# Kernel tuning notes

Hardware: AMD Instinct MI355X
Metric: run time of the kernel (lower is better)

## Reference

```python
import jax, jax.numpy as jnp
import numpy as np

N, E, F, H = 50000, 1_600_000, 6, 64


def setup_inputs() -> dict:
    key = jax.random.key(0)
    ks = jax.random.split(key, 12)
    inp = {
        "vertex_features": jax.random.normal(ks[0], (N, F), dtype=jnp.float32),
        "edges": jax.random.randint(ks[1], (2, E), 0, N, dtype=jnp.int64 if jax.config.jax_enable_x64 else jnp.int32),
        "weights": jax.random.uniform(ks[2], (E,), dtype=jnp.float32),
        # GCNConv layer params (glorot-ish scale) + biases (PyG default bias=True)
        "W1": jax.random.normal(ks[3], (F, H), dtype=jnp.float32) / np.sqrt(F),
        "b1": jnp.zeros((H,), jnp.float32),
        "W2": jax.random.normal(ks[4], (H, H), dtype=jnp.float32) / np.sqrt(H),
        "b2": jnp.zeros((H,), jnp.float32),
        "W3": jax.random.normal(ks[5], (H, H), dtype=jnp.float32) / np.sqrt(H),
        "b3": jnp.zeros((H,), jnp.float32),
        "Wl": jax.random.normal(ks[6], (H, 1), dtype=jnp.float32) / np.sqrt(H),
        "bl": jnp.zeros((1,), jnp.float32),
    }
    return inp


def _gcn_norm(edges, weights, n):
    # PyG gcn_norm: add self loops (weight 1), symmetric D^-1/2 A D^-1/2;
    # degree computed at target nodes (edge_index[1], flow source_to_target).
    row, col = edges[0], edges[1]
    loop = jnp.arange(n, dtype=row.dtype)
    row_f = jnp.concatenate([row, loop])
    col_f = jnp.concatenate([col, loop])
    w_f = jnp.concatenate([weights, jnp.ones((n,), weights.dtype)])
    deg = jax.ops.segment_sum(w_f, col_f, num_segments=n)
    dis = jnp.where(deg > 0, jax.lax.rsqrt(jnp.maximum(deg, 1e-30)), 0.0)
    norm = dis[row_f] * w_f * dis[col_f]
    return row_f, col_f, norm


def _gcn_conv(x, W, b, row, col, norm, n):
    xw = x @ W                                   # [n, H_out]
    agg = jax.ops.segment_sum(norm[:, None] * xw[row], col, num_segments=n)
    return agg + b


def reference(vertex_features, edges, weights, W1, b1, W2, b2, W3, b3, Wl, bl):
    n = vertex_features.shape[0]
    row, col, norm = _gcn_norm(edges, weights, n)  # norm identical for all layers
    h = jax.nn.sigmoid(_gcn_conv(vertex_features, W1, b1, row, col, norm, n))
    h = jax.nn.sigmoid(_gcn_conv(h, W2, b2, row, col, norm, n))
    h = jax.nn.sigmoid(_gcn_conv(h, W3, b3, row, col, norm, n))
    logits = h @ Wl + bl                           # [n, 1]
    return jax.nn.softmax(logits, axis=0)          # softmax over node dim
```

## Files before the change

### kernel.cpp

```cpp
#include <hip/hip_runtime.h>
#include <math.h>


#define BLK 256
#define SKB 256
#define CHUNK 4096

typedef __attribute__((ext_vector_type(8))) short bf16x8;
typedef __attribute__((ext_vector_type(4))) float f32x4;

__device__ inline unsigned short f2bf(float f) {
  unsigned u = __float_as_uint(f);
  return (unsigned short)((u + 0x7FFF + ((u >> 16) & 1)) >> 16);
}
__device__ inline float bflo(unsigned u) { return __uint_as_float(u << 16); }
__device__ inline float bfhi(unsigned u) { return __uint_as_float(u & 0xFFFF0000u); }


__global__ __launch_bounds__(256) void k_binscatter(
    const int* __restrict__ row, const int* __restrict__ col,
    const float* __restrict__ w, int E,
    int* __restrict__ bfill, int2* __restrict__ bucket, int CAP) {
  __shared__ int2 stage[CHUNK];
  __shared__ int lhist[SKB], lbase[SKB], gbase[SKB], lfill[SKB];
  int t = threadIdx.x;
  int e0 = blockIdx.x * CHUNK;
  int n = E - e0; if (n > CHUNK) n = CHUNK;
  lhist[t] = 0; lfill[t] = 0;
  __syncthreads();
  for (int i = t; i < n; i += BLK) atomicAdd(&lhist[((unsigned)col[e0 + i]) >> 8], 1);
  __syncthreads();
  lbase[t] = lhist[t];
  __syncthreads();
  for (int off = 1; off < SKB; off <<= 1) {
    int v = (t >= off) ? lbase[t - off] : 0;
    __syncthreads();
    lbase[t] += v;
    __syncthreads();
  }
  int excl = lbase[t] - lhist[t];
  int cb = lhist[t];
  gbase[t] = cb ? atomicAdd(&bfill[t << 4], cb) : 0;
  __syncthreads();
  lbase[t] = excl;
  __syncthreads();
  for (int i = t; i < n; i += BLK) {
    int c = col[e0 + i];
    int b = ((unsigned)c) >> 8;
    int r = atomicAdd(&lfill[b], 1);
    stage[lbase[b] + r] = make_int2(row[e0 + i] | (c << 16), __float_as_int(w[e0 + i]));
  }
  __syncthreads();
  for (int i = t; i < n; i += BLK) {
    int2 p = stage[i];
    int b = ((unsigned)p.x) >> 24;
    bucket[(size_t)b * CAP + gbase[b] + (i - lbase[b])] = p;
  }
}


__global__ __launch_bounds__(256) void k_build(
    const int2* __restrict__ bucket, const int* __restrict__ bfill,
    const float* __restrict__ x,
    unsigned* __restrict__ csr, int* __restrict__ cnt, int* __restrict__ start,
    float* __restrict__ dis, float* __restrict__ x8p, int CAP, int N) {
  __shared__ int   hist[SKB];
  __shared__ float wsum[SKB];
  __shared__ int   lstart[SKB + 1];
  __shared__ int   lfill[SKB];
  int b = blockIdx.x, t = threadIdx.x;
  int n0 = b << 8;
  int M = N - n0; if (M > 256) M = 256;
  if (M <= 0) return;
  hist[t] = 0; wsum[t] = 0.0f; lfill[t] = 0;
  __syncthreads();
  const int2* bb = bucket + (size_t)b * CAP;
  int ec = bfill[b << 4];
  for (int i = t; i < ec; i += BLK) {
    int2 p = bb[i];
    int lc = (((unsigned)p.x) >> 16) & 255;
    atomicAdd(&hist[lc], 1);
    atomicAdd(&wsum[lc], __int_as_float(p.y));
  }
  __syncthreads();
  if (t == 0) {
    int run = 0;
    for (int i = 0; i < M; ++i) { lstart[i] = run; run += hist[i]; }
    lstart[M] = run;
  }
  __syncthreads();
  if (t < M) {
    int n = n0 + t;
    cnt[n] = hist[t];
    start[n] = b * CAP + lstart[t];
    float d = 1.0f / sqrtf(wsum[t] + 1.0f);
    dis[n] = d;
    const float* xr = x + (size_t)n * 6;
    float* xo = x8p + (size_t)n * 8;
#pragma unroll
    for (int k = 0; k < 6; ++k) xo[k] = d * xr[k];
    xo[6] = 0.0f; xo[7] = 0.0f;
  }
  __syncthreads();
  for (int i = t; i < ec; i += BLK) {
    int2 p = bb[i];
    int lc = (((unsigned)p.x) >> 16) & 255;
    int pos = lstart[lc] + atomicAdd(&lfill[lc], 1);
    csr[(size_t)b * CAP + pos] =
        ((unsigned)p.x & 0xFFFFu) | ((unsigned)f2bf(__int_as_float(p.y)) << 16);
  }
}


__global__ void k_wprep(const float* __restrict__ W2, const float* __restrict__ W3,
                        unsigned short* __restrict__ W2b, unsigned short* __restrict__ W3b) {
  int i = blockIdx.x * blockDim.x + threadIdx.x;
  if (i < 4096) { W2b[i] = f2bf(W2[i]); W3b[i] = f2bf(W3[i]); }
}


__global__ void k_layer1(const float* __restrict__ x8p,
                         const int* __restrict__ start, const int* __restrict__ cnt,
                         const unsigned* __restrict__ csr, const float* __restrict__ dis,
                         const float* __restrict__ W1, const float* __restrict__ b1,
                         unsigned short* __restrict__ hb, int N) {
  int n = blockIdx.x * blockDim.x + threadIdx.x;
  if (n >= N) return;
  const float4* xr = (const float4*)(x8p + (size_t)n * 8);
  float4 lo = xr[0], hi = xr[1];
  int s = start[n], e = s + cnt[n];
  for (int i = s; i < e; ++i) {
    unsigned pe = csr[i];
    float v = bfhi(pe);
    const float4* sr = (const float4*)(x8p + (size_t)(pe & 0xFFFFu) * 8);
    float4 a = sr[0], b = sr[1];
    lo.x += v * a.x; lo.y += v * a.y; lo.z += v * a.z; lo.w += v * a.w;
    hi.x += v * b.x; hi.y += v * b.y;
  }
  float d = dis[n];
  float a0 = d * lo.x, a1 = d * lo.y, a2 = d * lo.z, a3 = d * lo.w;
  float a4 = d * hi.x, a5 = d * hi.y;
  unsigned short* o = hb + (size_t)n * 64;
#pragma unroll
  for (int j4 = 0; j4 < 16; ++j4) {
    float4 acc = *(const float4*)(b1 + j4 * 4);
    const float* Wc = W1 + j4 * 4;
    acc.x += a0*Wc[0] + a1*Wc[64] + a2*Wc[128] + a3*Wc[192] + a4*Wc[256] + a5*Wc[320];
    acc.y += a0*Wc[1] + a1*Wc[65] + a2*Wc[129] + a3*Wc[193] + a4*Wc[257] + a5*Wc[321];
    acc.z += a0*Wc[2] + a1*Wc[66] + a2*Wc[130] + a3*Wc[194] + a4*Wc[258] + a5*Wc[322];
    acc.w += a0*Wc[3] + a1*Wc[67] + a2*Wc[131] + a3*Wc[195] + a4*Wc[259] + a5*Wc[323];
    uint2 pk;
    pk.x = (unsigned)f2bf(d / (1.0f + expf(-acc.x))) |
           ((unsigned)f2bf(d / (1.0f + expf(-acc.y))) << 16);
    pk.y = (unsigned)f2bf(d / (1.0f + expf(-acc.z))) |
           ((unsigned)f2bf(d / (1.0f + expf(-acc.w))) << 16);
    *(uint2*)(o + j4 * 4) = pk;
  }
}


__global__ void k_agg64(const unsigned short* __restrict__ hb,
                        const int* __restrict__ start, const int* __restrict__ cnt,
                        const unsigned* __restrict__ csr, const float* __restrict__ dis,
                        unsigned short* __restrict__ aggb, int N) {
  int t = blockIdx.x * blockDim.x + threadIdx.x;
  int n = t >> 3, sub = t & 7;
  if (n >= N) return;
  uint4 sv = *(const uint4*)(hb + (size_t)n * 64 + sub * 8);
  float a0 = bflo(sv.x), a1 = bfhi(sv.x), a2 = bflo(sv.y), a3 = bfhi(sv.y);
  float a4 = bflo(sv.z), a5 = bfhi(sv.z), a6 = bflo(sv.w), a7 = bfhi(sv.w);
  int s = start[n], e = s + cnt[n];
  for (int i = s; i < e; ++i) {
    unsigned pe = csr[i];
    float v = bfhi(pe);
    uint4 hv = *(const uint4*)(hb + (size_t)(pe & 0xFFFFu) * 64 + sub * 8);
    a0 += v * bflo(hv.x); a1 += v * bfhi(hv.x);
    a2 += v * bflo(hv.y); a3 += v * bfhi(hv.y);
    a4 += v * bflo(hv.z); a5 += v * bfhi(hv.z);
    a6 += v * bflo(hv.w); a7 += v * bfhi(hv.w);
  }
  float d = dis[n];
  uint4 pk;
  pk.x = (unsigned)f2bf(d * a0) | ((unsigned)f2bf(d * a1) << 16);
  pk.y = (unsigned)f2bf(d * a2) | ((unsigned)f2bf(d * a3) << 16);
  pk.z = (unsigned)f2bf(d * a4) | ((unsigned)f2bf(d * a5) << 16);
  pk.w = (unsigned)f2bf(d * a6) | ((unsigned)f2bf(d * a7) << 16);
  *(uint4*)(aggb + (size_t)n * 64 + sub * 8) = pk;
}


__global__ __launch_bounds__(256) void k_dense64_mfma(
    const unsigned short* __restrict__ aggb, const unsigned short* __restrict__ Wb,
    const float* __restrict__ b, const float* __restrict__ dis,
    unsigned short* __restrict__ hb, int NS) {
  int wid = threadIdx.x >> 6, lane = threadIdx.x & 63;
  int quad = lane >> 4, r16 = lane & 15;
  bf16x8 Bf[2][4];
#pragma unroll
  for (int kt = 0; kt < 2; ++kt)
#pragma unroll
    for (int jt = 0; jt < 4; ++jt)
#pragma unroll
      for (int j = 0; j < 8; ++j)
        Bf[kt][jt][j] = (short)Wb[(kt * 32 + quad * 8 + j) * 64 + jt * 16 + r16];
  float bias[4];
#pragma unroll
  for (int jt = 0; jt < 4; ++jt) bias[jt] = b[jt * 16 + r16];
  int stride = gridDim.x * 4;
  for (int s = blockIdx.x * 4 + wid; s < NS; s += stride) {
    int n0 = s * 16;
    bf16x8 Af0 = *(const bf16x8*)(aggb + (size_t)(n0 + r16) * 64 + quad * 8);
    bf16x8 Af1 = *(const bf16x8*)(aggb + (size_t)(n0 + r16) * 64 + 32 + quad * 8);
    f32x4 C[4];
#pragma unroll
    for (int jt = 0; jt < 4; ++jt) {
      f32x4 z = {0.f, 0.f, 0.f, 0.f};
      z = __builtin_amdgcn_mfma_f32_16x16x32_bf16(Af0, Bf[0][jt], z, 0, 0, 0);
      z = __builtin_amdgcn_mfma_f32_16x16x32_bf16(Af1, Bf[1][jt], z, 0, 0, 0);
      C[jt] = z;
    }
    float dv[4];
#pragma unroll
    for (int reg = 0; reg < 4; ++reg) dv[reg] = dis[n0 + quad * 4 + reg];
#pragma unroll
    for (int jt = 0; jt < 4; ++jt)
#pragma unroll
      for (int reg = 0; reg < 4; ++reg) {
        float h = dv[reg] / (1.0f + expf(-(C[jt][reg] + bias[jt])));
        hb[(size_t)(n0 + quad * 4 + reg) * 64 + jt * 16 + r16] = f2bf(h);
      }
  }
}


__global__ __launch_bounds__(256) void k_head_mfma(
    const unsigned short* __restrict__ aggb, const unsigned short* __restrict__ Wb,
    const float* __restrict__ b, const float* __restrict__ Wl,
    const float* __restrict__ bl, float* __restrict__ expv,
    float* __restrict__ red_part, int NS) {
  int wid = threadIdx.x >> 6, lane = threadIdx.x & 63;
  int quad = lane >> 4, r16 = lane & 15;
  bf16x8 Bf[2][4];
#pragma unroll
  for (int kt = 0; kt < 2; ++kt)
#pragma unroll
    for (int jt = 0; jt < 4; ++jt)
#pragma unroll
      for (int j = 0; j < 8; ++j)
        Bf[kt][jt][j] = (short)Wb[(kt * 32 + quad * 8 + j) * 64 + jt * 16 + r16];
  float bias[4], wlv[4];
#pragma unroll
  for (int jt = 0; jt < 4; ++jt) {
    bias[jt] = b[jt * 16 + r16];
    wlv[jt]  = Wl[jt * 16 + r16];
  }
  float bl0 = bl[0];
  float lsum = 0.0f;
  int stride = gridDim.x * 4;
  for (int s = blockIdx.x * 4 + wid; s < NS; s += stride) {
    int n0 = s * 16;
    bf16x8 Af0 = *(const bf16x8*)(aggb + (size_t)(n0 + r16) * 64 + quad * 8);
    bf16x8 Af1 = *(const bf16x8*)(aggb + (size_t)(n0 + r16) * 64 + 32 + quad * 8);
    f32x4 C[4];
#pragma unroll
    for (int jt = 0; jt < 4; ++jt) {
      f32x4 z = {0.f, 0.f, 0.f, 0.f};
      z = __builtin_amdgcn_mfma_f32_16x16x32_bf16(Af0, Bf[0][jt], z, 0, 0, 0);
      z = __builtin_amdgcn_mfma_f32_16x16x32_bf16(Af1, Bf[1][jt], z, 0, 0, 0);
      C[jt] = z;
    }
    float p0 = 0, p1 = 0, p2 = 0, p3 = 0;
#pragma unroll
    for (int jt = 0; jt < 4; ++jt) {
      p0 += wlv[jt] / (1.0f + expf(-(C[jt][0] + bias[jt])));
      p1 += wlv[jt] / (1.0f + expf(-(C[jt][1] + bias[jt])));
      p2 += wlv[jt] / (1.0f + expf(-(C[jt][2] + bias[jt])));
      p3 += wlv[jt] / (1.0f + expf(-(C[jt][3] + bias[jt])));
    }
#pragma unroll
    for (int m = 1; m < 16; m <<= 1) {
      p0 += __shfl_xor(p0, m, 64);
      p1 += __shfl_xor(p1, m, 64);
      p2 += __shfl_xor(p2, m, 64);
      p3 += __shfl_xor(p3, m, 64);
    }
    float ls = 0.0f;
    if (r16 == 0) {
      float e0 = expf(p0 + bl0), e1 = expf(p1 + bl0);
      float e2 = expf(p2 + bl0), e3 = expf(p3 + bl0);
      int r = n0 + quad * 4;
      expv[r] = e0; expv[r + 1] = e1; expv[r + 2] = e2; expv[r + 3] = e3;
      ls = e0 + e1 + e2 + e3;
    }
    ls += __shfl_xor(ls, 16, 64);
    ls += __shfl_xor(ls, 32, 64);
    lsum += ls;
  }
  if (lane == 0) atomicAdd(&red_part[(blockIdx.x & 63) << 4], lsum);
}

__global__ void k_out(const float* __restrict__ expv, int N,
                      const float* __restrict__ red_part, float* __restrict__ out) {
  int i = blockIdx.x * blockDim.x + threadIdx.x;
  int lane = threadIdx.x & 63;
  float s = red_part[lane << 4];
#pragma unroll
  for (int o = 32; o > 0; o >>= 1) s += __shfl_down(s, o, 64);
  s = __shfl(s, 0, 64);
  if (i < N) out[i] = expv[i] / s;
}


extern "C" void kernel_launch(void* const* d_in, const int* in_sizes, int n_in,
                              void* d_out, int out_size, void* d_ws, size_t ws_size,
                              hipStream_t stream) {
  const float* x   = (const float*)d_in[0];
  const int*   edg = (const int*)d_in[1];
  const float* w   = (const float*)d_in[2];
  const float* W1  = (const float*)d_in[3];
  const float* b1  = (const float*)d_in[4];
  const float* W2  = (const float*)d_in[5];
  const float* b2  = (const float*)d_in[6];
  const float* W3  = (const float*)d_in[7];
  const float* b3  = (const float*)d_in[8];
  const float* Wl  = (const float*)d_in[9];
  const float* bl  = (const float*)d_in[10];
  float* out = (float*)d_out;

  const int N = in_sizes[0] / 6;
  const int E = in_sizes[2];
  const int* row = edg;
  const int* col = edg + E;
  const int NB = (N + 255) >> 8;
  const int NS = (N + 15) / 16;

  size_t off = 0;
  char* base = (char*)d_ws;
  auto alloc = [&](size_t bytes) -> void* {
    void* p = base + off;
    off += (bytes + 255) & ~(size_t)255;
    return p;
  };
  int*   bfill    = (int*)alloc((size_t)SKB * 16 * 4);
  float* red_part = (float*)alloc((size_t)64 * 16 * 4);
  size_t zero_bytes = off;
  int*   cnt    = (int*)alloc((size_t)N * 4);
  int*   start  = (int*)alloc((size_t)N * 4);
  float* dis    = (float*)alloc((size_t)N * 4);
  float* x8p    = (float*)alloc((size_t)N * 8 * 4);
  float* expv   = (float*)alloc((size_t)N * 4);
  unsigned short* hb  = (unsigned short*)alloc((size_t)N * 64 * 2);
  unsigned short* W2b = (unsigned short*)alloc(4096 * 2);
  unsigned short* W3b = (unsigned short*)alloc(4096 * 2);
  size_t remain = (ws_size > off) ? (ws_size - off) : 0;
  size_t aggsz = (size_t)N * 64 * 2;
  long long capn = ((long long)remain) / ((long long)NB * 12);
  int CAP = (int)capn;
  if (CAP > 9216) CAP = 9216;
  if (CAP < 8704) CAP = 8704;
  unsigned* csr = (unsigned*)alloc((size_t)NB * CAP * 4);
  size_t bksz = (size_t)NB * CAP * 8;
  void* shared_blk = alloc(aggsz > bksz ? aggsz : bksz);
  int2*           bucket = (int2*)shared_blk;
  unsigned short* aggb   = (unsigned short*)shared_blk;

  const int gE  = (E + CHUNK - 1) / CHUNK;
  const int gN  = (N + BLK - 1) / BLK;
  const int gN8 = (N * 8 + BLK - 1) / BLK;
  const int gM  = 200;

  hipMemsetAsync(d_ws, 0, zero_bytes, stream);

  k_wprep     <<<16, BLK, 0, stream>>>(W2, W3, W2b, W3b);
  k_binscatter<<<gE, BLK, 0, stream>>>(row, col, w, E, bfill, bucket, CAP);
  k_build     <<<NB, BLK, 0, stream>>>(bucket, bfill, x, csr, cnt, start, dis, x8p, CAP, N);

  k_layer1<<<gN, BLK, 0, stream>>>(x8p, start, cnt, csr, dis, W1, b1, hb, N);

  k_agg64      <<<gN8, BLK, 0, stream>>>(hb, start, cnt, csr, dis, aggb, N);
  k_dense64_mfma<<<gM, BLK, 0, stream>>>(aggb, W2b, b2, dis, hb, NS);

  k_agg64    <<<gN8, BLK, 0, stream>>>(hb, start, cnt, csr, dis, aggb, N);
  k_head_mfma<<<gM, BLK, 0, stream>>>(aggb, W3b, b3, Wl, bl, expv, red_part, NS);

  k_out<<<gN, BLK, 0, stream>>>(expv, N, red_part, out);
}
```

Baseline: 263.6 us.

## Fuse aggregation with MFMA dense layers via LDS tiles; store layer-1 features in bf16

Merges the per-layer neighbour aggregation and the MFMA dense transform into one kernel per layer. Each block aggregates 64 nodes into an LDS tile, then runs MFMA on that tile, so the intermediate aggregated buffer no longer goes through global memory and two launches are removed. Layer-2 output is written into the bucket buffer, which is free once the CSR is built. The layer-1 input features are also packed as bf16 to halve gather traffic, at some cost in precision. The dense kernels lose their persistent grid-stride loop and reload weight fragments in every block.

```diff
diff --git a/kernel.cpp b/kernel.cpp
--- a/kernel.cpp
+++ b/kernel.cpp
@@ -5,6 +5,7 @@
 #define BLK 256
 #define SKB 256
 #define CHUNK 4096
+#define LROW 72
 
 typedef __attribute__((ext_vector_type(8))) short bf16x8;
 typedef __attribute__((ext_vector_type(4))) float f32x4;
@@ -63,7 +64,7 @@
     const int2* __restrict__ bucket, const int* __restrict__ bfill,
     const float* __restrict__ x,
     unsigned* __restrict__ csr, int* __restrict__ cnt, int* __restrict__ start,
-    float* __restrict__ dis, float* __restrict__ x8p, int CAP, int N) {
+    float* __restrict__ dis, unsigned short* __restrict__ x8b, int CAP, int N) {
   __shared__ int   hist[SKB];
   __shared__ float wsum[SKB];
   __shared__ int   lstart[SKB + 1];
@@ -96,10 +97,12 @@
     float d = 1.0f / sqrtf(wsum[t] + 1.0f);
     dis[n] = d;
     const float* xr = x + (size_t)n * 6;
-    float* xo = x8p + (size_t)n * 8;
-#pragma unroll
-    for (int k = 0; k < 6; ++k) xo[k] = d * xr[k];
-    xo[6] = 0.0f; xo[7] = 0.0f;
+    uint4 pk;
+    pk.x = (unsigned)f2bf(d * xr[0]) | ((unsigned)f2bf(d * xr[1]) << 16);
+    pk.y = (unsigned)f2bf(d * xr[2]) | ((unsigned)f2bf(d * xr[3]) << 16);
+    pk.z = (unsigned)f2bf(d * xr[4]) | ((unsigned)f2bf(d * xr[5]) << 16);
+    pk.w = 0u;
+    *(uint4*)(x8b + (size_t)n * 8) = pk;
   }
   __syncthreads();
   for (int i = t; i < ec; i += BLK) {
@@ -119,27 +122,27 @@
 }
 
 
-__global__ void k_layer1(const float* __restrict__ x8p,
+__global__ void k_layer1(const unsigned short* __restrict__ x8b,
                          const int* __restrict__ start, const int* __restrict__ cnt,
                          const unsigned* __restrict__ csr, const float* __restrict__ dis,
                          const float* __restrict__ W1, const float* __restrict__ b1,
                          unsigned short* __restrict__ hb, int N) {
   int n = blockIdx.x * blockDim.x + threadIdx.x;
   if (n >= N) return;
-  const float4* xr = (const float4*)(x8p + (size_t)n * 8);
-  float4 lo = xr[0], hi = xr[1];
+  uint4 sv = *(const uint4*)(x8b + (size_t)n * 8);
+  float a0 = bflo(sv.x), a1 = bfhi(sv.x), a2 = bflo(sv.y);
+  float a3 = bfhi(sv.y), a4 = bflo(sv.z), a5 = bfhi(sv.z);
   int s = start[n], e = s + cnt[n];
   for (int i = s; i < e; ++i) {
     unsigned pe = csr[i];
     float v = bfhi(pe);
-    const float4* sr = (const float4*)(x8p + (size_t)(pe & 0xFFFFu) * 8);
-    float4 a = sr[0], b = sr[1];
-    lo.x += v * a.x; lo.y += v * a.y; lo.z += v * a.z; lo.w += v * a.w;
-    hi.x += v * b.x; hi.y += v * b.y;
+    uint4 hv = *(const uint4*)(x8b + (size_t)(pe & 0xFFFFu) * 8);
+    a0 += v * bflo(hv.x); a1 += v * bfhi(hv.x);
+    a2 += v * bflo(hv.y); a3 += v * bfhi(hv.y);
+    a4 += v * bflo(hv.z); a5 += v * bfhi(hv.z);
   }
   float d = dis[n];
-  float a0 = d * lo.x, a1 = d * lo.y, a2 = d * lo.z, a3 = d * lo.w;
-  float a4 = d * hi.x, a5 = d * hi.y;
+  a0 *= d; a1 *= d; a2 *= d; a3 *= d; a4 *= d; a5 *= d;
   unsigned short* o = hb + (size_t)n * 64;
 #pragma unroll
   for (int j4 = 0; j4 < 16; ++j4) {
@@ -159,41 +162,53 @@
 }
 
 
-__global__ void k_agg64(const unsigned short* __restrict__ hb,
-                        const int* __restrict__ start, const int* __restrict__ cnt,
-                        const unsigned* __restrict__ csr, const float* __restrict__ dis,
-                        unsigned short* __restrict__ aggb, int N) {
-  int t = blockIdx.x * blockDim.x + threadIdx.x;
-  int n = t >> 3, sub = t & 7;
-  if (n >= N) return;
-  uint4 sv = *(const uint4*)(hb + (size_t)n * 64 + sub * 8);
-  float a0 = bflo(sv.x), a1 = bfhi(sv.x), a2 = bflo(sv.y), a3 = bfhi(sv.y);
-  float a4 = bflo(sv.z), a5 = bfhi(sv.z), a6 = bflo(sv.w), a7 = bfhi(sv.w);
-  int s = start[n], e = s + cnt[n];
-  for (int i = s; i < e; ++i) {
-    unsigned pe = csr[i];
-    float v = bfhi(pe);
-    uint4 hv = *(const uint4*)(hb + (size_t)(pe & 0xFFFFu) * 64 + sub * 8);
-    a0 += v * bflo(hv.x); a1 += v * bfhi(hv.x);
-    a2 += v * bflo(hv.y); a3 += v * bfhi(hv.y);
-    a4 += v * bflo(hv.z); a5 += v * bfhi(hv.z);
-    a6 += v * bflo(hv.w); a7 += v * bfhi(hv.w);
-  }
-  float d = dis[n];
-  uint4 pk;
-  pk.x = (unsigned)f2bf(d * a0) | ((unsigned)f2bf(d * a1) << 16);
-  pk.y = (unsigned)f2bf(d * a2) | ((unsigned)f2bf(d * a3) << 16);
-  pk.z = (unsigned)f2bf(d * a4) | ((unsigned)f2bf(d * a5) << 16);
-  pk.w = (unsigned)f2bf(d * a6) | ((unsigned)f2bf(d * a7) << 16);
-  *(uint4*)(aggb + (size_t)n * 64 + sub * 8) = pk;
-}
-
-
-__global__ __launch_bounds__(256) void k_dense64_mfma(
-    const unsigned short* __restrict__ aggb, const unsigned short* __restrict__ Wb,
-    const float* __restrict__ b, const float* __restrict__ dis,
-    unsigned short* __restrict__ hb, int NS) {
-  int wid = threadIdx.x >> 6, lane = threadIdx.x & 63;
+__device__ inline void agg_tile(const unsigned short* __restrict__ hb,
+                                const int* __restrict__ start,
+                                const int* __restrict__ cnt,
+                                const unsigned* __restrict__ csr,
+                                const float* __restrict__ dis,
+                                unsigned short* lag, int n0, int N) {
+  int t = threadIdx.x;
+  int g = t >> 3, sub = t & 7;
+#pragma unroll
+  for (int rep = 0; rep < 2; ++rep) {
+    int r = rep * 32 + g;
+    int n = n0 + r;
+    uint4 pk = make_uint4(0u, 0u, 0u, 0u);
+    if (n < N) {
+      uint4 sv = *(const uint4*)(hb + (size_t)n * 64 + sub * 8);
+      float a0 = bflo(sv.x), a1 = bfhi(sv.x), a2 = bflo(sv.y), a3 = bfhi(sv.y);
+      float a4 = bflo(sv.z), a5 = bfhi(sv.z), a6 = bflo(sv.w), a7 = bfhi(sv.w);
+      int s = start[n], e = s + cnt[n];
+      for (int i = s; i < e; ++i) {
+        unsigned pe = csr[i];
+        float v = bfhi(pe);
+        uint4 hv = *(const uint4*)(hb + (size_t)(pe & 0xFFFFu) * 64 + sub * 8);
+        a0 += v * bflo(hv.x); a1 += v * bfhi(hv.x);
+        a2 += v * bflo(hv.y); a3 += v * bfhi(hv.y);
+        a4 += v * bflo(hv.z); a5 += v * bfhi(hv.z);
+        a6 += v * bflo(hv.w); a7 += v * bfhi(hv.w);
+      }
+      float d = dis[n];
+      pk.x = (unsigned)f2bf(d * a0) | ((unsigned)f2bf(d * a1) << 16);
+      pk.y = (unsigned)f2bf(d * a2) | ((unsigned)f2bf(d * a3) << 16);
+      pk.z = (unsigned)f2bf(d * a4) | ((unsigned)f2bf(d * a5) << 16);
+      pk.w = (unsigned)f2bf(d * a6) | ((unsigned)f2bf(d * a7) << 16);
+    }
+    *(uint4*)(lag + r * LROW + sub * 8) = pk;
+  }
+}
+
+
+__global__ __launch_bounds__(256) void k_layer2(
+    const unsigned short* __restrict__ hb_in,
+    const int* __restrict__ start, const int* __restrict__ cnt,
+    const unsigned* __restrict__ csr, const float* __restrict__ dis,
+    const unsigned short* __restrict__ Wb, const float* __restrict__ b,
+    unsigned short* __restrict__ hb_out, int N) {
+  __shared__ unsigned short lag[64 * LROW];
+  int t = threadIdx.x;
+  int wid = t >> 6, lane = t & 63;
   int quad = lane >> 4, r16 = lane & 15;
   bf16x8 Bf[2][4];
 #pragma unroll
@@ -206,39 +221,44 @@
   float bias[4];
 #pragma unroll
   for (int jt = 0; jt < 4; ++jt) bias[jt] = b[jt * 16 + r16];
-  int stride = gridDim.x * 4;
-  for (int s = blockIdx.x * 4 + wid; s < NS; s += stride) {
-    int n0 = s * 16;
-    bf16x8 Af0 = *(const bf16x8*)(aggb + (size_t)(n0 + r16) * 64 + quad * 8);
-    bf16x8 Af1 = *(const bf16x8*)(aggb + (size_t)(n0 + r16) * 64 + 32 + quad * 8);
-    f32x4 C[4];
-#pragma unroll
-    for (int jt = 0; jt < 4; ++jt) {
-      f32x4 z = {0.f, 0.f, 0.f, 0.f};
-      z = __builtin_amdgcn_mfma_f32_16x16x32_bf16(Af0, Bf[0][jt], z, 0, 0, 0);
-      z = __builtin_amdgcn_mfma_f32_16x16x32_bf16(Af1, Bf[1][jt], z, 0, 0, 0);
-      C[jt] = z;
+
+  int n0 = blockIdx.x * 64;
+  agg_tile(hb_in, start, cnt, csr, dis, lag, n0, N);
+  __syncthreads();
+
+  const unsigned short* arow = lag + (wid * 16 + r16) * LROW;
+  bf16x8 Af0 = *(const bf16x8*)(arow + quad * 8);
+  bf16x8 Af1 = *(const bf16x8*)(arow + 32 + quad * 8);
+  int nb = n0 + wid * 16 + quad * 4;
+  float dv[4];
+#pragma unroll
+  for (int reg = 0; reg < 4; ++reg) dv[reg] = (nb + reg < N) ? dis[nb + reg] : 0.f;
+#pragma unroll
+  for (int jt = 0; jt < 4; ++jt) {
+    f32x4 z = {0.f, 0.f, 0.f, 0.f};
+    z = __builtin_amdgcn_mfma_f32_16x16x32_bf16(Af0, Bf[0][jt], z, 0, 0, 0);
+    z = __builtin_amdgcn_mfma_f32_16x16x32_bf16(Af1, Bf[1][jt], z, 0, 0, 0);
+#pragma unroll
+    for (int reg = 0; reg < 4; ++reg) {
+      if (nb + reg < N) {
+        float h = dv[reg] / (1.0f + expf(-(z[reg] + bias[jt])));
+        hb_out[(size_t)(nb + reg) * 64 + jt * 16 + r16] = f2bf(h);
+      }
     }
-    float dv[4];
-#pragma unroll
-    for (int reg = 0; reg < 4; ++reg) dv[reg] = dis[n0 + quad * 4 + reg];
-#pragma unroll
-    for (int jt = 0; jt < 4; ++jt)
-#pragma unroll
-      for (int reg = 0; reg < 4; ++reg) {
-        float h = dv[reg] / (1.0f + expf(-(C[jt][reg] + bias[jt])));
-        hb[(size_t)(n0 + quad * 4 + reg) * 64 + jt * 16 + r16] = f2bf(h);
-      }
-  }
-}
-
-
-__global__ __launch_bounds__(256) void k_head_mfma(
-    const unsigned short* __restrict__ aggb, const unsigned short* __restrict__ Wb,
-    const float* __restrict__ b, const float* __restrict__ Wl,
-    const float* __restrict__ bl, float* __restrict__ expv,
-    float* __restrict__ red_part, int NS) {
-  int wid = threadIdx.x >> 6, lane = threadIdx.x & 63;
+  }
+}
+
+
+__global__ __launch_bounds__(256) void k_layer3(
+    const unsigned short* __restrict__ hb_in,
+    const int* __restrict__ start, const int* __restrict__ cnt,
+    const unsigned* __restrict__ csr, const float* __restrict__ dis,
+    const unsigned short* __restrict__ Wb, const float* __restrict__ b,
+    const float* __restrict__ Wl, const float* __restrict__ bl,
+    float* __restrict__ expv, float* __restrict__ red_part, int N) {
+  __shared__ unsigned short lag[64 * LROW];
+  int t = threadIdx.x;
+  int wid = t >> 6, lane = t & 63;
   int quad = lane >> 4, r16 = lane & 15;
   bf16x8 Bf[2][4];
 #pragma unroll
@@ -255,48 +275,44 @@
     wlv[jt]  = Wl[jt * 16 + r16];
   }
   float bl0 = bl[0];
-  float lsum = 0.0f;
-  int stride = gridDim.x * 4;
-  for (int s = blockIdx.x * 4 + wid; s < NS; s += stride) {
-    int n0 = s * 16;
-    bf16x8 Af0 = *(const bf16x8*)(aggb + (size_t)(n0 + r16) * 64 + quad * 8);
-    bf16x8 Af1 = *(const bf16x8*)(aggb + (size_t)(n0 + r16) * 64 + 32 + quad * 8);
-    f32x4 C[4];
-#pragma unroll
-    for (int jt = 0; jt < 4; ++jt) {
-      f32x4 z = {0.f, 0.f, 0.f, 0.f};
-      z = __builtin_amdgcn_mfma_f32_16x16x32_bf16(Af0, Bf[0][jt], z, 0, 0, 0);
-      z = __builtin_amdgcn_mfma_f32_16x16x32_bf16(Af1, Bf[1][jt], z, 0, 0, 0);
-      C[jt] = z;
+
+  int n0 = blockIdx.x * 64;
+  agg_tile(hb_in, start, cnt, csr, dis, lag, n0, N);
+  __syncthreads();
+
+  const unsigned short* arow = lag + (wid * 16 + r16) * LROW;
+  bf16x8 Af0 = *(const bf16x8*)(arow + quad * 8);
+  bf16x8 Af1 = *(const bf16x8*)(arow + 32 + quad * 8);
+  float p[4] = {0.f, 0.f, 0.f, 0.f};
+#pragma unroll
+  for (int jt = 0; jt < 4; ++jt) {
+    f32x4 z = {0.f, 0.f, 0.f, 0.f};
+    z = __builtin_amdgcn_mfma_f32_16x16x32_bf16(Af0, Bf[0][jt], z, 0, 0, 0);
+    z = __builtin_amdgcn_mfma_f32_16x16x32_bf16(Af1, Bf[1][jt], z, 0, 0, 0);
+#pragma unroll
+    for (int reg = 0; reg < 4; ++reg)
+      p[reg] += wlv[jt] / (1.0f + expf(-(z[reg] + bias[jt])));
+  }
+#pragma unroll
+  for (int m = 1; m < 16; m <<= 1) {
+#pragma unroll
+    for (int reg = 0; reg < 4; ++reg) p[reg] += __shfl_xor(p[reg], m, 64);
+  }
+  float ls = 0.0f;
+  if (r16 == 0) {
+    int nb = n0 + wid * 16 + quad * 4;
+#pragma unroll
+    for (int reg = 0; reg < 4; ++reg) {
+      if (nb + reg < N) {
+        float ev = expf(p[reg] + bl0);
+        expv[nb + reg] = ev;
+        ls += ev;
+      }
     }
-    float p0 = 0, p1 = 0, p2 = 0, p3 = 0;
-#pragma unroll
-    for (int jt = 0; jt < 4; ++jt) {
-      p0 += wlv[jt] / (1.0f + expf(-(C[jt][0] + bias[jt])));
-      p1 += wlv[jt] / (1.0f + expf(-(C[jt][1] + bias[jt])));
-      p2 += wlv[jt] / (1.0f + expf(-(C[jt][2] + bias[jt])));
-      p3 += wlv[jt] / (1.0f + expf(-(C[jt][3] + bias[jt])));
-    }
-#pragma unroll
-    for (int m = 1; m < 16; m <<= 1) {
-      p0 += __shfl_xor(p0, m, 64);
-      p1 += __shfl_xor(p1, m, 64);
-      p2 += __shfl_xor(p2, m, 64);
-      p3 += __shfl_xor(p3, m, 64);
-    }
-    float ls = 0.0f;
-    if (r16 == 0) {
-      float e0 = expf(p0 + bl0), e1 = expf(p1 + bl0);
-      float e2 = expf(p2 + bl0), e3 = expf(p3 + bl0);
-      int r = n0 + quad * 4;
-      expv[r] = e0; expv[r + 1] = e1; expv[r + 2] = e2; expv[r + 3] = e3;
-      ls = e0 + e1 + e2 + e3;
-    }
-    ls += __shfl_xor(ls, 16, 64);
-    ls += __shfl_xor(ls, 32, 64);
-    lsum += ls;
-  }
-  if (lane == 0) atomicAdd(&red_part[(blockIdx.x & 63) << 4], lsum);
+  }
+  ls += __shfl_xor(ls, 16, 64);
+  ls += __shfl_xor(ls, 32, 64);
+  if (lane == 0) atomicAdd(&red_part[(blockIdx.x & 63) << 4], ls);
 }
 
 __global__ void k_out(const float* __restrict__ expv, int N,
@@ -332,7 +348,6 @@
   const int* row = edg;
   const int* col = edg + E;
   const int NB = (N + 255) >> 8;
-  const int NS = (N + 15) / 16;
 
   size_t off = 0;
   char* base = (char*)d_ws;
@@ -347,41 +362,36 @@
   int*   cnt    = (int*)alloc((size_t)N * 4);
   int*   start  = (int*)alloc((size_t)N * 4);
   float* dis    = (float*)alloc((size_t)N * 4);
-  float* x8p    = (float*)alloc((size_t)N * 8 * 4);
   float* expv   = (float*)alloc((size_t)N * 4);
+  unsigned short* x8b = (unsigned short*)alloc((size_t)N * 8 * 2);
   unsigned short* hb  = (unsigned short*)alloc((size_t)N * 64 * 2);
   unsigned short* W2b = (unsigned short*)alloc(4096 * 2);
   unsigned short* W3b = (unsigned short*)alloc(4096 * 2);
   size_t remain = (ws_size > off) ? (ws_size - off) : 0;
-  size_t aggsz = (size_t)N * 64 * 2;
   long long capn = ((long long)remain) / ((long long)NB * 12);
   int CAP = (int)capn;
   if (CAP > 9216) CAP = 9216;
   if (CAP < 8704) CAP = 8704;
-  unsigned* csr = (unsigned*)alloc((size_t)NB * CAP * 4);
-  size_t bksz = (size_t)NB * CAP * 8;
-  void* shared_blk = alloc(aggsz > bksz ? aggsz : bksz);
-  int2*           bucket = (int2*)shared_blk;
-  unsigned short* aggb   = (unsigned short*)shared_blk;
-
-  const int gE  = (E + CHUNK - 1) / CHUNK;
-  const int gN  = (N + BLK - 1) / BLK;
-  const int gN8 = (N * 8 + BLK - 1) / BLK;
-  const int gM  = 200;
+  unsigned* csr  = (unsigned*)alloc((size_t)NB * CAP * 4);
+  int2*     bucket = (int2*)alloc((size_t)NB * CAP * 8);
+
+  const int gE   = (E + CHUNK - 1) / CHUNK;
+  const int gN   = (N + BLK - 1) / BLK;
+  const int g64  = (N + 63) / 64;
 
   hipMemsetAsync(d_ws, 0, zero_bytes, stream);
 
   k_wprep     <<<16, BLK, 0, stream>>>(W2, W3, W2b, W3b);
   k_binscatter<<<gE, BLK, 0, stream>>>(row, col, w, E, bfill, bucket, CAP);
-  k_build     <<<NB, BLK, 0, stream>>>(bucket, bfill, x, csr, cnt, start, dis, x8p, CAP, N);
-
-  k_layer1<<<gN, BLK, 0, stream>>>(x8p, start, cnt, csr, dis, W1, b1, hb, N);
-
-  k_agg64      <<<gN8, BLK, 0, stream>>>(hb, start, cnt, csr, dis, aggb, N);
-  k_dense64_mfma<<<gM, BLK, 0, stream>>>(aggb, W2b, b2, dis, hb, NS);
-
-  k_agg64    <<<gN8, BLK, 0, stream>>>(hb, start, cnt, csr, dis, aggb, N);
-  k_head_mfma<<<gM, BLK, 0, stream>>>(aggb, W3b, b3, Wl, bl, expv, red_part, NS);
+  k_build     <<<NB, BLK, 0, stream>>>(bucket, bfill, x, csr, cnt, start, dis, x8b, CAP, N);
+
+  k_layer1<<<gN, BLK, 0, stream>>>(x8b, start, cnt, csr, dis, W1, b1, hb, N);
+
+  k_layer2<<<g64, BLK, 0, stream>>>(hb, start, cnt, csr, dis, W2b, b2,
+                                    (unsigned short*)bucket, N);
+
+  k_layer3<<<g64, BLK, 0, stream>>>((unsigned short*)bucket, start, cnt, csr, dis,
+                                    W3b, b3, Wl, bl, expv, red_part, N);
 
   k_out<<<gN, BLK, 0, stream>>>(expv, N, red_part, out);
 }
```

New measurement: 292.3 us. 10.9% more time.
